# Kernel optimization log

Measured on AMD Instinct MI355X. Metric: run time of the kernel, lower is better.

## Reference

```python
import jax, jax.numpy as jnp
import numpy as np

B, N, F, S, M, K = 32, 4096, 256, 256, 1024, 11
EPS = 1e-06  # slot-attention epsilon
LN_EPS = 1e-05  # torch LayerNorm default
NUM_ITERS = 3


def _ln(x, g, b):
    mu = jnp.mean(x, axis=-1, keepdims=True)
    var = jnp.mean(jnp.square(x - mu), axis=-1, keepdims=True)
    return (x - mu) * jax.lax.rsqrt(var + LN_EPS) * g + b


def setup_inputs() -> dict:
    key = jax.random.key(0)
    ks = jax.random.split(key, 12)
    def xavier(k, shape):
        fan_in, fan_out = shape[0], shape[-1]
        lim = np.sqrt(6.0 / (fan_in + fan_out))
        return jax.random.uniform(k, shape, jnp.float32, -lim, lim)
    return {
        "features": jax.random.normal(ks[0], (B, N, F), jnp.float32),
        "sigma": jnp.array([0.1], jnp.float32),
        "z": jax.random.normal(ks[1], (B, K, S), jnp.float32),
        "slots_init_w": xavier(ks[2], (K, S)),
        "gf": jnp.ones((F,), jnp.float32), "bf": jnp.zeros((F,), jnp.float32),
        "gs": jnp.ones((S,), jnp.float32), "bs": jnp.zeros((S,), jnp.float32),
        "gm": jnp.ones((S,), jnp.float32), "bm": jnp.zeros((S,), jnp.float32),
        "Wk": xavier(ks[3], (F, S)),
        "Wv": xavier(ks[4], (F, S)),
        "Wq": xavier(ks[5], (S, S)),
        "W_ih": xavier(ks[6], (3 * S, S)),
        "W_hh": xavier(ks[7], (3 * S, S)),
        "b_ih": jnp.zeros((3 * S,), jnp.float32),
        "b_hh": jnp.zeros((3 * S,), jnp.float32),
        "W1": xavier(ks[8], (S, M)), "b1": jnp.zeros((M,), jnp.float32),
        "W2": xavier(ks[9], (M, S)), "b2": jnp.zeros((S,), jnp.float32),
    }


def _gru(x, h, W_ih, W_hh, b_ih, b_hh):
    # torch GRUCell: gates ordered (r, z, n)
    gi = x @ W_ih.T + b_ih  # [..., 3S]
    gh = h @ W_hh.T + b_hh
    ir, iz, inn = jnp.split(gi, 3, axis=-1)
    hr, hz, hn = jnp.split(gh, 3, axis=-1)
    r = jax.nn.sigmoid(ir + hr)
    zg = jax.nn.sigmoid(iz + hz)
    n = jnp.tanh(inn + r * hn)
    return (1.0 - zg) * n + zg * h


def reference(features, sigma, z, slots_init_w, gf, bf, gs, bs, gm, bm,
              Wk, Wv, Wq, W_ih, W_hh, b_ih, b_hh, W1, b1, W2, b2):
    mu = jnp.broadcast_to(slots_init_w[None], (features.shape[0], K, S))
    slots_init = mu + z * sigma * jax.lax.stop_gradient(mu)
    feats = _ln(features, gf, bf)
    k = feats @ Wk  # [B,N,S]
    v = feats @ Wv  # [B,N,S]
    D = v.shape[-1]
    scale = D ** -0.5
    slots = slots_init
    attn = None
    for i in range(NUM_ITERS):
        if i == NUM_ITERS - 1:
            slots = jax.lax.stop_gradient(slots) + slots_init - jax.lax.stop_gradient(slots_init)
        slots_prev = slots
        q = _ln(slots, gs, bs) @ Wq  # [B,K,S]
        attn_logits = jnp.einsum('bid,bjd->bij', q, k) * scale  # [B,K,N]
        attn = jax.nn.softmax(attn_logits, axis=1)  # softmax over slots axis
        attn_wm = attn / (jnp.sum(attn, axis=-1, keepdims=True) + EPS)
        updates = jnp.einsum('bij,bjd->bid', attn_wm, v)  # [B,K,S]
        slots = _gru(updates, slots_prev, W_ih, W_hh, b_ih, b_hh)
        slots = slots + (jax.nn.relu(_ln(slots, gm, bm) @ W1 + b1) @ W2 + b2)
    return slots, attn
```

## Files before the change

### kernel.cpp

```cpp
#include <hip/hip_runtime.h>

#define EPS 1e-6f
#define LN_EPS 1e-5f

typedef unsigned short u16;
typedef unsigned int u32;
typedef short bf16x8 __attribute__((ext_vector_type(8)));
typedef float f32x4 __attribute__((ext_vector_type(4)));

__device__ __forceinline__ float bf2f(u16 u) {
  return __uint_as_float(((u32)u) << 16);
}
__device__ __forceinline__ u16 f2bf(float f) {
  u32 x = __float_as_uint(f);
  x += 0x7fffu + ((x >> 16) & 1u);
  return (u16)(x >> 16);
}

__global__ void prep_kernel(const float* __restrict__ W_ih,
                            const float* __restrict__ W_hh,
                            const float* __restrict__ W1,
                            const float* __restrict__ W2,
                            const float* __restrict__ Wq,
                            const float* __restrict__ Wk,
                            const float* __restrict__ Wv,
                            const float* __restrict__ slots_init_w,
                            const float* __restrict__ z,
                            const float* __restrict__ sigma,
                            float* __restrict__ wihT, float* __restrict__ whhT,
                            short* __restrict__ W1b, short* __restrict__ W2b,
                            short* __restrict__ Wqb, short* __restrict__ Btb,
                            float* __restrict__ slots, float* __restrict__ upd,
                            float* __restrict__ sums) {
  int e = blockIdx.x * 256 + threadIdx.x;
  if (e < 196608) {
    int j = e >> 8, d = e & 255;
    wihT[d * 768 + j] = W_ih[e];
  } else if (e < 393216) {
    int e2 = e - 196608;
    int j = e2 >> 8, d = e2 & 255;
    whhT[d * 768 + j] = W_hh[e2];
  } else if (e < 655360) {
    int e2 = e - 393216;
    W1b[e2] = (short)f2bf(W1[e2]);
  } else if (e < 917504) {
    int e2 = e - 655360;
    W2b[e2] = (short)f2bf(W2[e2]);
  } else if (e < 983040) {
    int e2 = e - 917504;
    Wqb[e2] = (short)f2bf(Wq[e2]);
  } else if (e < 1114112) {
    int e2 = e - 983040;
    int f = e2 >> 9, j = e2 & 511;
    float v = (j < 256) ? Wk[f * 256 + j] : Wv[f * 256 + (j - 256)];
    Btb[j * 256 + f] = (short)f2bf(v);
  } else if (e < 1204224) {
    int i = e - 1114112;
    int s = i & 255;
    int k = (i >> 8) % 11;
    float wv = slots_init_w[k * 256 + s];
    slots[i] = wv + z[i] * sigma[0] * wv;
    upd[i] = 0.f;
    if (i < 352) sums[i] = 0.f;
  }
}

__global__ __launch_bounds__(256) void gemm_kv(
    const float* __restrict__ feat, const short* __restrict__ Btb,
    const float* __restrict__ gf, const float* __restrict__ bfp,
    short* __restrict__ knorm, short* __restrict__ vT) {
  __shared__ short As[16384];
  __shared__ short Bs[2][8192];
  int t = threadIdx.x;
  int w = t >> 6, lane = t & 63;
  int quad = lane >> 4, l16 = lane & 15;
  int i0 = blockIdx.x * 64;
  int wi = (w & 1) * 32, wj = (w >> 1) * 64;

  {
    #pragma unroll
    for (int c = 0; c < 4; ++c) {
      int lin = c * 256 + t;
      int jr = lin >> 3, p = lin & 7;
      int q = (p - jr) & 7;
      const short* gB = Btb + (long)jr * 256 + q * 8;
      __builtin_amdgcn_global_load_lds(
          (const __attribute__((address_space(1))) void*)gB,
          (__attribute__((address_space(3))) void*)&Bs[0][lin * 8], 16, 0, 0);
    }
  }

  {
    int r = t >> 2;
    int qd = t & 3;
    const float* frow = feat + (long)(i0 + r) * 256 + qd * 64;
    float4 fv[16];
    float s = 0.f, s2 = 0.f;
    #pragma unroll
    for (int i = 0; i < 16; ++i) {
      fv[i] = *(const float4*)(frow + i * 4);
      s += fv[i].x + fv[i].y + fv[i].z + fv[i].w;
      s2 += fv[i].x * fv[i].x + fv[i].y * fv[i].y + fv[i].z * fv[i].z +
            fv[i].w * fv[i].w;
    }
    s += __shfl_xor(s, 1); s2 += __shfl_xor(s2, 1);
    s += __shfl_xor(s, 2); s2 += __shfl_xor(s2, 2);
    float mu = s * (1.f / 256.f);
    float rs = rsqrtf(s2 * (1.f / 256.f) - mu * mu + LN_EPS);
    #pragma unroll
    for (int c = 0; c < 8; ++c) {
      float4 a = fv[c * 2], b = fv[c * 2 + 1];
      int fb = qd * 64 + c * 8;
      float4 g0 = *(const float4*)(gf + fb);
      float4 g1 = *(const float4*)(gf + fb + 4);
      float4 e0 = *(const float4*)(bfp + fb);
      float4 e1 = *(const float4*)(bfp + fb + 4);
      bf16x8 pk;
      pk[0] = (short)f2bf((a.x - mu) * rs * g0.x + e0.x);
      pk[1] = (short)f2bf((a.y - mu) * rs * g0.y + e0.y);
      pk[2] = (short)f2bf((a.z - mu) * rs * g0.z + e0.z);
      pk[3] = (short)f2bf((a.w - mu) * rs * g0.w + e0.w);
      pk[4] = (short)f2bf((b.x - mu) * rs * g1.x + e1.x);
      pk[5] = (short)f2bf((b.y - mu) * rs * g1.y + e1.y);
      pk[6] = (short)f2bf((b.z - mu) * rs * g1.z + e1.z);
      pk[7] = (short)f2bf((b.w - mu) * rs * g1.w + e1.w);
      int p = qd * 8 + ((c + 2 * qd + r) & 7);
      *(bf16x8*)&As[r * 256 + p * 8] = pk;
    }
  }
  __syncthreads();

  f32x4 acc[2][4];
  #pragma unroll
  for (int a = 0; a < 2; ++a)
    #pragma unroll
    for (int b = 0; b < 4; ++b) acc[a][b] = (f32x4){0.f, 0.f, 0.f, 0.f};

  for (int idx = 0; idx < 16; ++idx) {
    int jq = idx >> 2, ks = idx & 3;
    int buf = idx & 1;
    if (idx < 15) {
      int jn = (idx + 1) >> 2, kn = (idx + 1) & 3;
      #pragma unroll
      for (int c = 0; c < 4; ++c) {
        int lin = c * 256 + t;
        int jr = lin >> 3, p = lin & 7;
        int q = (p - jr) & 7;
        const short* gB = Btb + (long)(jn * 128 + jr) * 256 + kn * 64 + q * 8;
        __builtin_amdgcn_global_load_lds(
            (const __attribute__((address_space(1))) void*)gB,
            (__attribute__((address_space(3))) void*)&Bs[buf ^ 1][lin * 8],
            16, 0, 0);
      }
    }
    #pragma unroll
    for (int kh = 0; kh < 2; ++kh) {
      bf16x8 af[2], bfr[4];
      #pragma unroll
      for (int mi = 0; mi < 2; ++mi) {
        int m = wi + mi * 16 + l16;
        int p = ks * 8 + ((kh * 4 + quad + 2 * ks + m) & 7);
        af[mi] = *(const bf16x8*)&As[m * 256 + p * 8];
      }
      #pragma unroll
      for (int ni = 0; ni < 4; ++ni) {
        int j = wj + ni * 16 + l16;
        int p = ((kh * 4 + quad) + j) & 7;
        bfr[ni] = *(const bf16x8*)&Bs[buf][j * 64 + p * 8];
      }
      if (jq < 2) {
        #pragma unroll
        for (int mi = 0; mi < 2; ++mi)
          #pragma unroll
          for (int ni = 0; ni < 4; ++ni)
            acc[mi][ni] = __builtin_amdgcn_mfma_f32_16x16x32_bf16(
                bfr[ni], af[mi], acc[mi][ni], 0, 0, 0);
      } else {
        #pragma unroll
        for (int mi = 0; mi < 2; ++mi)
          #pragma unroll
          for (int ni = 0; ni < 4; ++ni)
            acc[mi][ni] = __builtin_amdgcn_mfma_f32_16x16x32_bf16(
                af[mi], bfr[ni], acc[mi][ni], 0, 0, 0);
      }
    }
    if (ks == 3) {
      if (jq < 2) {
        #pragma unroll
        for (int mi = 0; mi < 2; ++mi) {
          long i = i0 + wi + mi * 16 + l16;
          #pragma unroll
          for (int ni = 0; ni < 4; ++ni) {
            int fb = jq * 128 + wj + ni * 16 + quad * 4;
            ushort4 u;
            u.x = f2bf(acc[mi][ni][0]);
            u.y = f2bf(acc[mi][ni][1]);
            u.z = f2bf(acc[mi][ni][2]);
            u.w = f2bf(acc[mi][ni][3]);
            *(ushort4*)&knorm[i * 256 + fb] = u;
          }
        }
      } else {
        #pragma unroll
        for (int ni = 0; ni < 4; ++ni) {
          int s = (jq - 2) * 128 + wj + ni * 16 + l16;
          #pragma unroll
          for (int mi = 0; mi < 2; ++mi) {
            long ib = i0 + wi + mi * 16 + quad * 4;
            ushort4 u;
            u.x = f2bf(acc[mi][ni][0]);
            u.y = f2bf(acc[mi][ni][1]);
            u.z = f2bf(acc[mi][ni][2]);
            u.w = f2bf(acc[mi][ni][3]);
            *(ushort4*)&vT[(long)s * 131072 + ib] = u;
          }
        }
      }
      #pragma unroll
      for (int a = 0; a < 2; ++a)
        #pragma unroll
        for (int b = 0; b < 4; ++b) acc[a][b] = (f32x4){0.f, 0.f, 0.f, 0.f};
    }
    __syncthreads();
  }
}

__global__ __launch_bounds__(256) void qproj_kernel(
    const float* __restrict__ slots, const float* __restrict__ gs,
    const float* __restrict__ bs, const short* __restrict__ Wqb,
    float* __restrict__ qout) {
  __shared__ float lnq[256];
  __shared__ float red[8];
  int row = blockIdx.x, t = threadIdx.x;
  int w = t >> 6, lane = t & 63;
  float x = slots[(long)row * 256 + t];
  float s = x, s2 = x * x;
  #pragma unroll
  for (int off = 32; off > 0; off >>= 1) {
    s += __shfl_xor(s, off);
    s2 += __shfl_xor(s2, off);
  }
  if (lane == 0) { red[w * 2] = s; red[w * 2 + 1] = s2; }
  __syncthreads();
  float st = red[0] + red[2] + red[4] + red[6];
  float st2 = red[1] + red[3] + red[5] + red[7];
  float mu = st * (1.f / 256.f);
  float rs = rsqrtf(st2 * (1.f / 256.f) - mu * mu + LN_EPS);
  lnq[t] = (x - mu) * rs * gs[t] + bs[t];
  __syncthreads();
  float acc = 0.f;
  for (int k = 0; k < 256; ++k)
    acc += lnq[k] * bf2f((u16)Wqb[k * 256 + t]);
  qout[(long)row * 256 + t] = acc;
}

__global__ __launch_bounds__(256) void attn_upd(
    const float* __restrict__ q, const short* __restrict__ knorm,
    const short* __restrict__ vT, float* __restrict__ attn_out,
    float* __restrict__ sums, float* __restrict__ upd, int emit_attn) {
  __shared__ short qs[16 * 264];
  __shared__ short ps[16 * 520];
  int b = blockIdx.y;
  int n0 = blockIdx.x * 512;
  int t = threadIdx.x, lane = t & 63;
  int w = t >> 6, quad = lane >> 4, l16 = lane & 15;
  for (int e = t; e < 5 * 264; e += 256) qs[11 * 264 + e] = 0;
  for (int e = t; e < 2816; e += 256) {
    int kk = e >> 8, f = e & 255;
    qs[kk * 264 + f] = (short)f2bf(q[b * 2816 + e]);
  }
  __syncthreads();
  f32x4 acc[8];
  #pragma unroll
  for (int mi = 0; mi < 8; ++mi) acc[mi] = (f32x4){0.f, 0.f, 0.f, 0.f};
  long nbase = (long)b * 4096 + n0 + w * 128;
  const short* kb = knorm + (nbase + l16) * 256 + quad * 8;
  #pragma unroll
  for (int c = 0; c < 8; ++c) {
    bf16x8 qf = *(const bf16x8*)&qs[l16 * 264 + c * 32 + quad * 8];
    #pragma unroll
    for (int mi = 0; mi < 8; ++mi) {
      bf16x8 kf = *(const bf16x8*)&kb[mi * 16 * 256 + c * 32];
      acc[mi] = __builtin_amdgcn_mfma_f32_16x16x32_bf16(kf, qf, acc[mi], 0, 0, 0);
    }
  }
  bool valid = l16 < 11;
  float slsum = 0.f;
  #pragma unroll
  for (int mi = 0; mi < 8; ++mi) {
    float4 pv;
    #pragma unroll
    for (int r = 0; r < 4; ++r) {
      float L = acc[mi][r] * 0.0625f;
      float Lm = valid ? L : -1e30f;
      Lm = fmaxf(Lm, __shfl_xor(Lm, 1));
      Lm = fmaxf(Lm, __shfl_xor(Lm, 2));
      Lm = fmaxf(Lm, __shfl_xor(Lm, 4));
      Lm = fmaxf(Lm, __shfl_xor(Lm, 8));
      float p = valid ? expf(L - Lm) : 0.f;
      float ss = p;
      ss += __shfl_xor(ss, 1);
      ss += __shfl_xor(ss, 2);
      ss += __shfl_xor(ss, 4);
      ss += __shfl_xor(ss, 8);
      p = p / ss;
      (&pv.x)[r] = p;
      slsum += p;
      ps[l16 * 520 + w * 128 + mi * 16 + quad * 4 + r] = (short)f2bf(p);
    }
    if (emit_attn && valid)
      *(float4*)(attn_out + ((long)b * 11 + l16) * 4096 + n0 + w * 128 +
                 mi * 16 + quad * 4) = pv;
  }
  slsum += __shfl_xor(slsum, 16);
  slsum += __shfl_xor(slsum, 32);
  if (valid && quad == 0) atomicAdd(&sums[b * 11 + l16], slsum);
  __syncthreads();
  f32x4 acc4[4];
  #pragma unroll
  for (int mi = 0; mi < 4; ++mi) acc4[mi] = (f32x4){0.f, 0.f, 0.f, 0.f};
  #pragma unroll
  for (int kst = 0; kst < 16; ++kst) {
    int nb = kst * 32 + quad * 8;
    bf16x8 bps = *(const bf16x8*)&ps[l16 * 520 + nb];
    #pragma unroll
    for (int mi = 0; mi < 4; ++mi) {
      int s = (w * 4 + mi) * 16 + l16;
      bf16x8 av =
          *(const bf16x8*)&vT[(long)s * 131072 + (long)b * 4096 + n0 + nb];
      acc4[mi] =
          __builtin_amdgcn_mfma_f32_16x16x32_bf16(av, bps, acc4[mi], 0, 0, 0);
    }
  }
  if (l16 < 11) {
    #pragma unroll
    for (int mi = 0; mi < 4; ++mi) {
      int sb = (w * 4 + mi) * 16 + quad * 4;
      #pragma unroll
      for (int r = 0; r < 4; ++r)
        atomicAdd(&upd[((long)b * 11 + l16) * 256 + sb + r], acc4[mi][r]);
    }
  }
}

__global__ __launch_bounds__(256) void slot_step(
    float* __restrict__ upd, float* __restrict__ sums,
    const float* __restrict__ slots_in,
    const float* __restrict__ wihT, const float* __restrict__ whhT,
    const float* __restrict__ b_ih, const float* __restrict__ b_hh,
    const float* __restrict__ gm, const float* __restrict__ bm,
    const short* __restrict__ W1b, const float* __restrict__ b1,
    const short* __restrict__ W2b, const float* __restrict__ b2,
    const float* __restrict__ gs, const float* __restrict__ bs,
    const short* __restrict__ Wqb,
    float* __restrict__ slots_out, float* __restrict__ qout, int emit_q) {
  __shared__ float xs[2][256], hs[2][256], sgv[2][256], ln1[2][256];
  __shared__ float giv[2][768], ghv[2][768];
  __shared__ float h1v[2][1024];
  __shared__ float pw2[4][2][256];
  __shared__ float red[2][2];
  int t = threadIdx.x;
  int w = t >> 6, lane = t & 63;
  int r0 = blockIdx.x * 2;
  #pragma unroll
  for (int row = 0; row < 2; ++row) {
    int r = r0 + row;
    float sc = 1.0f / (sums[r] + EPS);
    xs[row][t] = upd[(long)r * 256 + t] * sc;
    hs[row][t] = slots_in[(long)r * 256 + t];
  }
  __syncthreads();
  #pragma unroll
  for (int row = 0; row < 2; ++row) {
    upd[(long)(r0 + row) * 256 + t] = 0.f;
    if (t == row) sums[r0 + row] = 0.f;
  }
  {
    float accI[2][3] = {}, accH[2][3] = {};
    for (int k = 0; k < 256; ++k) {
      float x0 = xs[0][k], x1 = xs[1][k];
      float h0 = hs[0][k], h1 = hs[1][k];
      #pragma unroll
      for (int j = 0; j < 3; ++j) {
        float wI = wihT[k * 768 + j * 256 + t];
        float wH = whhT[k * 768 + j * 256 + t];
        accI[0][j] += x0 * wI; accI[1][j] += x1 * wI;
        accH[0][j] += h0 * wH; accH[1][j] += h1 * wH;
      }
    }
    #pragma unroll
    for (int row = 0; row < 2; ++row)
      #pragma unroll
      for (int j = 0; j < 3; ++j) {
        giv[row][j * 256 + t] = accI[row][j] + b_ih[j * 256 + t];
        ghv[row][j * 256 + t] = accH[row][j] + b_hh[j * 256 + t];
      }
  }
  __syncthreads();
  #pragma unroll
  for (int row = 0; row < 2; ++row) {
    float irv = giv[row][t], izv = giv[row][256 + t], inv = giv[row][512 + t];
    float hrv = ghv[row][t], hzv = ghv[row][256 + t], hnv = ghv[row][512 + t];
    float hv = hs[row][t];
    float rg = 1.f / (1.f + expf(-(irv + hrv)));
    float zg = 1.f / (1.f + expf(-(izv + hzv)));
    float ng = tanhf(inv + rg * hnv);
    sgv[row][t] = (1.f - zg) * ng + zg * hv;
  }
  __syncthreads();
  if (w < 2) {
    float4 sv = *(const float4*)&sgv[w][lane * 4];
    float s = sv.x + sv.y + sv.z + sv.w;
    float s2 = sv.x * sv.x + sv.y * sv.y + sv.z * sv.z + sv.w * sv.w;
    #pragma unroll
    for (int off = 32; off > 0; off >>= 1) {
      s += __shfl_xor(s, off);
      s2 += __shfl_xor(s2, off);
    }
    if (lane == 0) {
      float mu = s * (1.f / 256.f);
      red[w][0] = mu;
      red[w][1] = rsqrtf(s2 * (1.f / 256.f) - mu * mu + LN_EPS);
    }
  }
  __syncthreads();
  #pragma unroll
  for (int row = 0; row < 2; ++row)
    ln1[row][t] = (sgv[row][t] - red[row][0]) * red[row][1] * gm[t] + bm[t];
  __syncthreads();
  {
    float acc1[2][4] = {};
    for (int k = 0; k < 256; ++k) {
      ushort4 w4 = *(const ushort4*)(W1b + (long)k * 1024 + 4 * t);
      float wv[4] = {bf2f(w4.x), bf2f(w4.y), bf2f(w4.z), bf2f(w4.w)};
      float l0 = ln1[0][k], l1 = ln1[1][k];
      #pragma unroll
      for (int j = 0; j < 4; ++j) {
        acc1[0][j] += l0 * wv[j];
        acc1[1][j] += l1 * wv[j];
      }
    }
    #pragma unroll
    for (int row = 0; row < 2; ++row)
      #pragma unroll
      for (int j = 0; j < 4; ++j)
        h1v[row][4 * t + j] = fmaxf(acc1[row][j] + b1[4 * t + j], 0.f);
  }
  __syncthreads();
  {
    float acc2[2][4] = {};
    int kbase = w * 256;
    for (int kk = 0; kk < 256; ++kk) {
      int k = kbase + kk;
      ushort4 w4 = *(const ushort4*)(W2b + (long)k * 256 + 4 * lane);
      float wv[4] = {bf2f(w4.x), bf2f(w4.y), bf2f(w4.z), bf2f(w4.w)};
      float h0 = h1v[0][k], h1 = h1v[1][k];
      #pragma unroll
      for (int j = 0; j < 4; ++j) {
        acc2[0][j] += h0 * wv[j];
        acc2[1][j] += h1 * wv[j];
      }
    }
    #pragma unroll
    for (int row = 0; row < 2; ++row)
      #pragma unroll
      for (int j = 0; j < 4; ++j) pw2[w][row][4 * lane + j] = acc2[row][j];
  }
  __syncthreads();
  float outv[2];
  #pragma unroll
  for (int row = 0; row < 2; ++row) {
    float s = pw2[0][row][t] + pw2[1][row][t] + pw2[2][row][t] + pw2[3][row][t];
    outv[row] = s + b2[t] + sgv[row][t];
    slots_out[(long)(r0 + row) * 256 + t] = outv[row];
  }
  if (emit_q) {
    __syncthreads();
    xs[0][t] = outv[0];
    xs[1][t] = outv[1];
    __syncthreads();
    if (w < 2) {
      float4 sv = *(const float4*)&xs[w][lane * 4];
      float s = sv.x + sv.y + sv.z + sv.w;
      float s2 = sv.x * sv.x + sv.y * sv.y + sv.z * sv.z + sv.w * sv.w;
      #pragma unroll
      for (int off = 32; off > 0; off >>= 1) {
        s += __shfl_xor(s, off);
        s2 += __shfl_xor(s2, off);
      }
      if (lane == 0) {
        float mu = s * (1.f / 256.f);
        red[w][0] = mu;
        red[w][1] = rsqrtf(s2 * (1.f / 256.f) - mu * mu + LN_EPS);
      }
    }
    __syncthreads();
    #pragma unroll
    for (int row = 0; row < 2; ++row)
      hs[row][t] = (xs[row][t] - red[row][0]) * red[row][1] * gs[t] + bs[t];
    __syncthreads();
    float accq[2] = {};
    for (int k = 0; k < 256; ++k) {
      float wq = bf2f((u16)Wqb[k * 256 + t]);
      accq[0] += hs[0][k] * wq;
      accq[1] += hs[1][k] * wq;
    }
    #pragma unroll
    for (int row = 0; row < 2; ++row)
      qout[(long)(r0 + row) * 256 + t] = accq[row];
  }
}

extern "C" void kernel_launch(void* const* d_in, const int* in_sizes, int n_in,
                              void* d_out, int out_size, void* d_ws,
                              size_t ws_size, hipStream_t stream) {
  const float* features = (const float*)d_in[0];
  const float* sigma = (const float*)d_in[1];
  const float* z = (const float*)d_in[2];
  const float* slots_init_w = (const float*)d_in[3];
  const float* gf = (const float*)d_in[4];
  const float* bf = (const float*)d_in[5];
  const float* gs = (const float*)d_in[6];
  const float* bs = (const float*)d_in[7];
  const float* gm = (const float*)d_in[8];
  const float* bm = (const float*)d_in[9];
  const float* Wk = (const float*)d_in[10];
  const float* Wv = (const float*)d_in[11];
  const float* Wq = (const float*)d_in[12];
  const float* W_ih = (const float*)d_in[13];
  const float* W_hh = (const float*)d_in[14];
  const float* b_ih = (const float*)d_in[15];
  const float* b_hh = (const float*)d_in[16];
  const float* W1 = (const float*)d_in[17];
  const float* b1 = (const float*)d_in[18];
  const float* W2 = (const float*)d_in[19];
  const float* b2 = (const float*)d_in[20];

  float* ws = (float*)d_ws;
  size_t o = 0;
  short* knorm = (short*)(ws + o); o += 16777216;
  short* vT = (short*)(ws + o); o += 16777216;
  short* Btb = (short*)(ws + o); o += 65536;
  float* wihT = ws + o; o += 196608;
  float* whhT = ws + o; o += 196608;
  short* W1b = (short*)(ws + o); o += 131072;
  short* W2b = (short*)(ws + o); o += 131072;
  short* Wqb = (short*)(ws + o); o += 32768;
  float* slots = ws + o; o += 90112;
  float* qbuf = ws + o; o += 90112;
  float* upd = ws + o; o += 90112;
  float* sums = ws + o; o += 352;

  float* out_slots = (float*)d_out;
  float* out_attn = (float*)d_out + 90112;

  prep_kernel<<<4704, 256, 0, stream>>>(W_ih, W_hh, W1, W2, Wq, Wk, Wv,
                                        slots_init_w, z, sigma, wihT, whhT,
                                        W1b, W2b, Wqb, Btb, slots, upd, sums);
  gemm_kv<<<2048, 256, 0, stream>>>(features, Btb, gf, bf, knorm, vT);
  qproj_kernel<<<352, 256, 0, stream>>>(slots, gs, bs, Wqb, qbuf);

  for (int it = 0; it < 3; ++it) {
    attn_upd<<<dim3(8, 32), 256, 0, stream>>>(
        qbuf, knorm, vT, out_attn, sums, upd, (it == 2) ? 1 : 0);
    slot_step<<<176, 256, 0, stream>>>(
        upd, sums, slots, wihT, whhT, b_ih, b_hh, gm, bm, W1b, b1, W2b, b2,
        gs, bs, Wqb, (it == 2) ? out_slots : slots, qbuf, (it < 2) ? 1 : 0);
  }
}
```

Baseline: 689.1 us.

## Stage K/V epilogue through LDS, fold q-projection into GEMM launch, bf16 GRU weights

The K/V GEMM epilogue now writes bf16 results into a padded LDS tile and then emits 16-byte coalesced global stores, replacing scattered 8-byte stores (notably the strided vT transpose writes). The separate q-projection kernel is removed; its work runs as 352 extra blocks of the gemm_kv launch, which saves one launch. GRU weight matrices are converted to bf16 to halve the weight bandwidth in slot_step, at some precision cost. The epilogue adds extra LDS and barriers per output tile.

```diff
diff --git a/kernel.cpp b/kernel.cpp
--- a/kernel.cpp
+++ b/kernel.cpp
@@ -27,7 +27,7 @@
                             const float* __restrict__ slots_init_w,
                             const float* __restrict__ z,
                             const float* __restrict__ sigma,
-                            float* __restrict__ wihT, float* __restrict__ whhT,
+                            short* __restrict__ wihTb, short* __restrict__ whhTb,
                             short* __restrict__ W1b, short* __restrict__ W2b,
                             short* __restrict__ Wqb, short* __restrict__ Btb,
                             float* __restrict__ slots, float* __restrict__ upd,
@@ -35,11 +35,11 @@
   int e = blockIdx.x * 256 + threadIdx.x;
   if (e < 196608) {
     int j = e >> 8, d = e & 255;
-    wihT[d * 768 + j] = W_ih[e];
+    wihTb[d * 768 + j] = (short)f2bf(W_ih[e]);
   } else if (e < 393216) {
     int e2 = e - 196608;
     int j = e2 >> 8, d = e2 & 255;
-    whhT[d * 768 + j] = W_hh[e2];
+    whhTb[d * 768 + j] = (short)f2bf(W_hh[e2]);
   } else if (e < 655360) {
     int e2 = e - 393216;
     W1b[e2] = (short)f2bf(W1[e2]);
@@ -68,12 +68,43 @@
 __global__ __launch_bounds__(256) void gemm_kv(
     const float* __restrict__ feat, const short* __restrict__ Btb,
     const float* __restrict__ gf, const float* __restrict__ bfp,
-    short* __restrict__ knorm, short* __restrict__ vT) {
+    short* __restrict__ knorm, short* __restrict__ vT,
+    const float* __restrict__ slots, const float* __restrict__ gs,
+    const float* __restrict__ bs, const short* __restrict__ Wqb,
+    float* __restrict__ qbuf) {
   __shared__ short As[16384];
   __shared__ short Bs[2][8192];
+  __shared__ short Cs[4608];
   int t = threadIdx.x;
   int w = t >> 6, lane = t & 63;
   int quad = lane >> 4, l16 = lane & 15;
+
+  if (blockIdx.x >= 2048) {
+    float* lnq = (float*)As;
+    float* red = (float*)As + 256;
+    int row = blockIdx.x - 2048;
+    float x = slots[(long)row * 256 + t];
+    float s = x, s2 = x * x;
+    #pragma unroll
+    for (int off = 32; off > 0; off >>= 1) {
+      s += __shfl_xor(s, off);
+      s2 += __shfl_xor(s2, off);
+    }
+    if (lane == 0) { red[w * 2] = s; red[w * 2 + 1] = s2; }
+    __syncthreads();
+    float st = red[0] + red[2] + red[4] + red[6];
+    float st2 = red[1] + red[3] + red[5] + red[7];
+    float mu = st * (1.f / 256.f);
+    float rs = rsqrtf(st2 * (1.f / 256.f) - mu * mu + LN_EPS);
+    lnq[t] = (x - mu) * rs * gs[t] + bs[t];
+    __syncthreads();
+    float acc = 0.f;
+    for (int k = 0; k < 256; ++k)
+      acc += lnq[k] * bf2f((u16)Wqb[k * 256 + t]);
+    qbuf[(long)row * 256 + t] = acc;
+    return;
+  }
+
   int i0 = blockIdx.x * 64;
   int wi = (w & 1) * 32, wj = (w >> 1) * 64;
 
@@ -187,33 +218,63 @@
     if (ks == 3) {
       if (jq < 2) {
         #pragma unroll
-        for (int mi = 0; mi < 2; ++mi) {
-          long i = i0 + wi + mi * 16 + l16;
+        for (int half = 0; half < 2; ++half) {
+          if ((w >> 1) == half) {
+            #pragma unroll
+            for (int mi = 0; mi < 2; ++mi) {
+              int il = wi + mi * 16 + l16;
+              #pragma unroll
+              for (int ni = 0; ni < 4; ++ni) {
+                int fw = ni * 16 + quad * 4;
+                ushort4 u;
+                u.x = f2bf(acc[mi][ni][0]);
+                u.y = f2bf(acc[mi][ni][1]);
+                u.z = f2bf(acc[mi][ni][2]);
+                u.w = f2bf(acc[mi][ni][3]);
+                *(ushort4*)&Cs[il * 72 + fw] = u;
+              }
+            }
+          }
+          __syncthreads();
           #pragma unroll
-          for (int ni = 0; ni < 4; ++ni) {
-            int fb = jq * 128 + wj + ni * 16 + quad * 4;
-            ushort4 u;
-            u.x = f2bf(acc[mi][ni][0]);
-            u.y = f2bf(acc[mi][ni][1]);
-            u.z = f2bf(acc[mi][ni][2]);
-            u.w = f2bf(acc[mi][ni][3]);
-            *(ushort4*)&knorm[i * 256 + fb] = u;
+          for (int c = 0; c < 2; ++c) {
+            int e = c * 256 + t;
+            int il = e >> 3, f8 = e & 7;
+            bf16x8 vv = *(const bf16x8*)&Cs[il * 72 + f8 * 8];
+            *(bf16x8*)&knorm[(long)(i0 + il) * 256 + jq * 128 + half * 64 +
+                             f8 * 8] = vv;
           }
+          __syncthreads();
         }
       } else {
         #pragma unroll
-        for (int ni = 0; ni < 4; ++ni) {
-          int s = (jq - 2) * 128 + wj + ni * 16 + l16;
+        for (int half = 0; half < 2; ++half) {
+          if ((w >> 1) == half) {
+            #pragma unroll
+            for (int ni = 0; ni < 4; ++ni) {
+              int sw = ni * 16 + l16;
+              #pragma unroll
+              for (int mi = 0; mi < 2; ++mi) {
+                int il = wi + mi * 16 + quad * 4;
+                ushort4 u;
+                u.x = f2bf(acc[mi][ni][0]);
+                u.y = f2bf(acc[mi][ni][1]);
+                u.z = f2bf(acc[mi][ni][2]);
+                u.w = f2bf(acc[mi][ni][3]);
+                *(ushort4*)&Cs[sw * 72 + il] = u;
+              }
+            }
+          }
+          __syncthreads();
           #pragma unroll
-          for (int mi = 0; mi < 2; ++mi) {
-            long ib = i0 + wi + mi * 16 + quad * 4;
-            ushort4 u;
-            u.x = f2bf(acc[mi][ni][0]);
-            u.y = f2bf(acc[mi][ni][1]);
-            u.z = f2bf(acc[mi][ni][2]);
-            u.w = f2bf(acc[mi][ni][3]);
-            *(ushort4*)&vT[(long)s * 131072 + ib] = u;
+          for (int c = 0; c < 2; ++c) {
+            int e = c * 256 + t;
+            int sl_ = e >> 3, i8 = e & 7;
+            bf16x8 vv = *(const bf16x8*)&Cs[sl_ * 72 + i8 * 8];
+            *(bf16x8*)&vT[(long)((jq - 2) * 128 + half * 64 + sl_) * 131072 +
+                          i0 + i8 * 8] = vv;
           }
+          __syncthreads();
         }
       }
       #pragma unroll
@@ -223,35 +284,6 @@
     }
     __syncthreads();
   }
-}
-
-__global__ __launch_bounds__(256) void qproj_kernel(
-    const float* __restrict__ slots, const float* __restrict__ gs,
-    const float* __restrict__ bs, const short* __restrict__ Wqb,
-    float* __restrict__ qout) {
-  __shared__ float lnq[256];
-  __shared__ float red[8];
-  int row = blockIdx.x, t = threadIdx.x;
-  int w = t >> 6, lane = t & 63;
-  float x = slots[(long)row * 256 + t];
-  float s = x, s2 = x * x;
-  #pragma unroll
-  for (int off = 32; off > 0; off >>= 1) {
-    s += __shfl_xor(s, off);
-    s2 += __shfl_xor(s2, off);
-  }
-  if (lane == 0) { red[w * 2] = s; red[w * 2 + 1] = s2; }
-  __syncthreads();
-  float st = red[0] + red[2] + red[4] + red[6];
-  float st2 = red[1] + red[3] + red[5] + red[7];
-  float mu = st * (1.f / 256.f);
-  float rs = rsqrtf(st2 * (1.f / 256.f) - mu * mu + LN_EPS);
-  lnq[t] = (x - mu) * rs * gs[t] + bs[t];
-  __syncthreads();
-  float acc = 0.f;
-  for (int k = 0; k < 256; ++k)
-    acc += lnq[k] * bf2f((u16)Wqb[k * 256 + t]);
-  qout[(long)row * 256 + t] = acc;
 }
 
 __global__ __launch_bounds__(256) void attn_upd(
@@ -346,7 +378,7 @@
 __global__ __launch_bounds__(256) void slot_step(
     float* __restrict__ upd, float* __restrict__ sums,
     const float* __restrict__ slots_in,
-    const float* __restrict__ wihT, const float* __restrict__ whhT,
+    const short* __restrict__ wihTb, const short* __restrict__ whhTb,
     const float* __restrict__ b_ih, const float* __restrict__ b_hh,
     const float* __restrict__ gm, const float* __restrict__ bm,
     const short* __restrict__ W1b, const float* __restrict__ b1,
@@ -382,8 +414,8 @@
       float h0 = hs[0][k], h1 = hs[1][k];
       #pragma unroll
       for (int j = 0; j < 3; ++j) {
-        float wI = wihT[k * 768 + j * 256 + t];
-        float wH = whhT[k * 768 + j * 256 + t];
+        float wI = bf2f((u16)wihTb[k * 768 + j * 256 + t]);
+        float wH = bf2f((u16)whhTb[k * 768 + j * 256 + t]);
         accI[0][j] += x0 * wI; accI[1][j] += x1 * wI;
         accH[0][j] += h0 * wH; accH[1][j] += h1 * wH;
       }
@@ -541,8 +573,8 @@
   short* knorm = (short*)(ws + o); o += 16777216;
   short* vT = (short*)(ws + o); o += 16777216;
   short* Btb = (short*)(ws + o); o += 65536;
-  float* wihT = ws + o; o += 196608;
-  float* whhT = ws + o; o += 196608;
+  short* wihTb = (short*)(ws + o); o += 98304;
+  short* whhTb = (short*)(ws + o); o += 98304;
   short* W1b = (short*)(ws + o); o += 131072;
   short* W2b = (short*)(ws + o); o += 131072;
   short* Wqb = (short*)(ws + o); o += 32768;
@@ -555,16 +587,16 @@
   float* out_attn = (float*)d_out + 90112;
 
   prep_kernel<<<4704, 256, 0, stream>>>(W_ih, W_hh, W1, W2, Wq, Wk, Wv,
-                                        slots_init_w, z, sigma, wihT, whhT,
+                                        slots_init_w, z, sigma, wihTb, whhTb,
                                         W1b, W2b, Wqb, Btb, slots, upd, sums);
-  gemm_kv<<<2048, 256, 0, stream>>>(features, Btb, gf, bf, knorm, vT);
-  qproj_kernel<<<352, 256, 0, stream>>>(slots, gs, bs, Wqb, qbuf);
+  gemm_kv<<<2400, 256, 0, stream>>>(features, Btb, gf, bf, knorm, vT,
+                                    slots, gs, bs, Wqb, qbuf);
 
   for (int it = 0; it < 3; ++it) {
     attn_upd<<<dim3(8, 32), 256, 0, stream>>>(
         qbuf, knorm, vT, out_attn, sums, upd, (it == 2) ? 1 : 0);
     slot_step<<<176, 256, 0, stream>>>(
-        upd, sums, slots, wihT, whhT, b_ih, b_hh, gm, bm, W1b, b1, W2b, b2,
+        upd, sums, slots, wihTb, whhTb, b_ih, b_hh, gm, bm, W1b, b1, W2b, b2,
         gs, bs, Wqb, (it == 2) ? out_slots : slots, qbuf, (it < 2) ? 1 : 0);
   }
 }
```

Result: slower. 804.1 us (+16.7%).

## Fuse q-projection into KV GEMM launch, split attn blocks finer, bf16 GRU weights

Applied to the files above, without the earlier changes.

Three changes. The q-projection kernel is folded into the KV GEMM launch as extra blocks, which removes one launch. attn_upd now covers 256 tokens per block instead of 512, doubling the grid to 512 blocks for better CU occupancy at the cost of more atomics. The transposed GRU weights are stored in bf16 to halve their load traffic in slot_step, which slightly reduces the precision of the GRU matmuls.

```diff
diff --git a/kernel.cpp b/kernel.cpp
--- a/kernel.cpp
+++ b/kernel.cpp
@@ -27,7 +27,7 @@
                             const float* __restrict__ slots_init_w,
                             const float* __restrict__ z,
                             const float* __restrict__ sigma,
-                            float* __restrict__ wihT, float* __restrict__ whhT,
+                            short* __restrict__ wihTb, short* __restrict__ whhTb,
                             short* __restrict__ W1b, short* __restrict__ W2b,
                             short* __restrict__ Wqb, short* __restrict__ Btb,
                             float* __restrict__ slots, float* __restrict__ upd,
@@ -35,11 +35,11 @@
   int e = blockIdx.x * 256 + threadIdx.x;
   if (e < 196608) {
     int j = e >> 8, d = e & 255;
-    wihT[d * 768 + j] = W_ih[e];
+    wihTb[d * 768 + j] = (short)f2bf(W_ih[e]);
   } else if (e < 393216) {
     int e2 = e - 196608;
     int j = e2 >> 8, d = e2 & 255;
-    whhT[d * 768 + j] = W_hh[e2];
+    whhTb[d * 768 + j] = (short)f2bf(W_hh[e2]);
   } else if (e < 655360) {
     int e2 = e - 393216;
     W1b[e2] = (short)f2bf(W1[e2]);
@@ -68,12 +68,42 @@
 __global__ __launch_bounds__(256) void gemm_kv(
     const float* __restrict__ feat, const short* __restrict__ Btb,
     const float* __restrict__ gf, const float* __restrict__ bfp,
-    short* __restrict__ knorm, short* __restrict__ vT) {
+    short* __restrict__ knorm, short* __restrict__ vT,
+    const float* __restrict__ slots, const float* __restrict__ gs,
+    const float* __restrict__ bs, const short* __restrict__ Wqb,
+    float* __restrict__ qbuf) {
   __shared__ short As[16384];
   __shared__ short Bs[2][8192];
   int t = threadIdx.x;
   int w = t >> 6, lane = t & 63;
   int quad = lane >> 4, l16 = lane & 15;
+
+  if (blockIdx.x >= 2048) {
+    float* lnq = (float*)As;
+    float* red = (float*)As + 256;
+    int row = blockIdx.x - 2048;
+    float x = slots[(long)row * 256 + t];
+    float s = x, s2 = x * x;
+    #pragma unroll
+    for (int off = 32; off > 0; off >>= 1) {
+      s += __shfl_xor(s, off);
+      s2 += __shfl_xor(s2, off);
+    }
+    if (lane == 0) { red[w * 2] = s; red[w * 2 + 1] = s2; }
+    __syncthreads();
+    float st = red[0] + red[2] + red[4] + red[6];
+    float st2 = red[1] + red[3] + red[5] + red[7];
+    float mu = st * (1.f / 256.f);
+    float rs = rsqrtf(st2 * (1.f / 256.f) - mu * mu + LN_EPS);
+    lnq[t] = (x - mu) * rs * gs[t] + bs[t];
+    __syncthreads();
+    float acc = 0.f;
+    for (int k = 0; k < 256; ++k)
+      acc += lnq[k] * bf2f((u16)Wqb[k * 256 + t]);
+    qbuf[(long)row * 256 + t] = acc;
+    return;
+  }
+
   int i0 = blockIdx.x * 64;
   int wi = (w & 1) * 32, wj = (w >> 1) * 64;
 
@@ -225,43 +255,14 @@
   }
 }
 
-__global__ __launch_bounds__(256) void qproj_kernel(
-    const float* __restrict__ slots, const float* __restrict__ gs,
-    const float* __restrict__ bs, const short* __restrict__ Wqb,
-    float* __restrict__ qout) {
-  __shared__ float lnq[256];
-  __shared__ float red[8];
-  int row = blockIdx.x, t = threadIdx.x;
-  int w = t >> 6, lane = t & 63;
-  float x = slots[(long)row * 256 + t];
-  float s = x, s2 = x * x;
-  #pragma unroll
-  for (int off = 32; off > 0; off >>= 1) {
-    s += __shfl_xor(s, off);
-    s2 += __shfl_xor(s2, off);
-  }
-  if (lane == 0) { red[w * 2] = s; red[w * 2 + 1] = s2; }
-  __syncthreads();
-  float st = red[0] + red[2] + red[4] + red[6];
-  float st2 = red[1] + red[3] + red[5] + red[7];
-  float mu = st * (1.f / 256.f);
-  float rs = rsqrtf(st2 * (1.f / 256.f) - mu * mu + LN_EPS);
-  lnq[t] = (x - mu) * rs * gs[t] + bs[t];
-  __syncthreads();
-  float acc = 0.f;
-  for (int k = 0; k < 256; ++k)
-    acc += lnq[k] * bf2f((u16)Wqb[k * 256 + t]);
-  qout[(long)row * 256 + t] = acc;
-}
-
 __global__ __launch_bounds__(256) void attn_upd(
     const float* __restrict__ q, const short* __restrict__ knorm,
     const short* __restrict__ vT, float* __restrict__ attn_out,
     float* __restrict__ sums, float* __restrict__ upd, int emit_attn) {
   __shared__ short qs[16 * 264];
-  __shared__ short ps[16 * 520];
+  __shared__ short ps[16 * 264];
   int b = blockIdx.y;
-  int n0 = blockIdx.x * 512;
+  int n0 = blockIdx.x * 256;
   int t = threadIdx.x, lane = t & 63;
   int w = t >> 6, quad = lane >> 4, l16 = lane & 15;
   for (int e = t; e < 5 * 264; e += 256) qs[11 * 264 + e] = 0;
@@ -270,16 +271,16 @@
     qs[kk * 264 + f] = (short)f2bf(q[b * 2816 + e]);
   }
   __syncthreads();
-  f32x4 acc[8];
-  #pragma unroll
-  for (int mi = 0; mi < 8; ++mi) acc[mi] = (f32x4){0.f, 0.f, 0.f, 0.f};
-  long nbase = (long)b * 4096 + n0 + w * 128;
+  f32x4 acc[4];
+  #pragma unroll
+  for (int mi = 0; mi < 4; ++mi) acc[mi] = (f32x4){0.f, 0.f, 0.f, 0.f};
+  long nbase = (long)b * 4096 + n0 + w * 64;
   const short* kb = knorm + (nbase + l16) * 256 + quad * 8;
   #pragma unroll
   for (int c = 0; c < 8; ++c) {
     bf16x8 qf = *(const bf16x8*)&qs[l16 * 264 + c * 32 + quad * 8];
     #pragma unroll
-    for (int mi = 0; mi < 8; ++mi) {
+    for (int mi = 0; mi < 4; ++mi) {
       bf16x8 kf = *(const bf16x8*)&kb[mi * 16 * 256 + c * 32];
       acc[mi] = __builtin_amdgcn_mfma_f32_16x16x32_bf16(kf, qf, acc[mi], 0, 0, 0);
     }
@@ -287,7 +288,7 @@
   bool valid = l16 < 11;
   float slsum = 0.f;
   #pragma unroll
-  for (int mi = 0; mi < 8; ++mi) {
+  for (int mi = 0; mi < 4; ++mi) {
     float4 pv;
     #pragma unroll
     for (int r = 0; r < 4; ++r) {
@@ -306,10 +307,10 @@
       p = p / ss;
       (&pv.x)[r] = p;
       slsum += p;
-      ps[l16 * 520 + w * 128 + mi * 16 + quad * 4 + r] = (short)f2bf(p);
+      ps[l16 * 264 + w * 64 + mi * 16 + quad * 4 + r] = (short)f2bf(p);
     }
     if (emit_attn && valid)
-      *(float4*)(attn_out + ((long)b * 11 + l16) * 4096 + n0 + w * 128 +
+      *(float4*)(attn_out + ((long)b * 11 + l16) * 4096 + n0 + w * 64 +
                  mi * 16 + quad * 4) = pv;
   }
   slsum += __shfl_xor(slsum, 16);
@@ -320,9 +321,9 @@
   #pragma unroll
   for (int mi = 0; mi < 4; ++mi) acc4[mi] = (f32x4){0.f, 0.f, 0.f, 0.f};
   #pragma unroll
-  for (int kst = 0; kst < 16; ++kst) {
+  for (int kst = 0; kst < 8; ++kst) {
     int nb = kst * 32 + quad * 8;
-    bf16x8 bps = *(const bf16x8*)&ps[l16 * 520 + nb];
+    bf16x8 bps = *(const bf16x8*)&ps[l16 * 264 + nb];
     #pragma unroll
     for (int mi = 0; mi < 4; ++mi) {
       int s = (w * 4 + mi) * 16 + l16;
@@ -346,7 +347,7 @@
 __global__ __launch_bounds__(256) void slot_step(
     float* __restrict__ upd, float* __restrict__ sums,
     const float* __restrict__ slots_in,
-    const float* __restrict__ wihT, const float* __restrict__ whhT,
+    const short* __restrict__ wihTb, const short* __restrict__ whhTb,
     const float* __restrict__ b_ih, const float* __restrict__ b_hh,
     const float* __restrict__ gm, const float* __restrict__ bm,
     const short* __restrict__ W1b, const float* __restrict__ b1,
@@ -382,8 +383,8 @@
       float h0 = hs[0][k], h1 = hs[1][k];
       #pragma unroll
       for (int j = 0; j < 3; ++j) {
-        float wI = wihT[k * 768 + j * 256 + t];
-        float wH = whhT[k * 768 + j * 256 + t];
+        float wI = bf2f((u16)wihTb[k * 768 + j * 256 + t]);
+        float wH = bf2f((u16)whhTb[k * 768 + j * 256 + t]);
         accI[0][j] += x0 * wI; accI[1][j] += x1 * wI;
         accH[0][j] += h0 * wH; accH[1][j] += h1 * wH;
       }
@@ -541,8 +542,8 @@
   short* knorm = (short*)(ws + o); o += 16777216;
   short* vT = (short*)(ws + o); o += 16777216;
   short* Btb = (short*)(ws + o); o += 65536;
-  float* wihT = ws + o; o += 196608;
-  float* whhT = ws + o; o += 196608;
+  short* wihTb = (short*)(ws + o); o += 98304;
+  short* whhTb = (short*)(ws + o); o += 98304;
   short* W1b = (short*)(ws + o); o += 131072;
   short* W2b = (short*)(ws + o); o += 131072;
   short* Wqb = (short*)(ws + o); o += 32768;
@@ -555,16 +556,16 @@
   float* out_attn = (float*)d_out + 90112;
 
   prep_kernel<<<4704, 256, 0, stream>>>(W_ih, W_hh, W1, W2, Wq, Wk, Wv,
-                                        slots_init_w, z, sigma, wihT, whhT,
+                                        slots_init_w, z, sigma, wihTb, whhTb,
                                         W1b, W2b, Wqb, Btb, slots, upd, sums);
-  gemm_kv<<<2048, 256, 0, stream>>>(features, Btb, gf, bf, knorm, vT);
-  qproj_kernel<<<352, 256, 0, stream>>>(slots, gs, bs, Wqb, qbuf);
+  gemm_kv<<<2400, 256, 0, stream>>>(features, Btb, gf, bf, knorm, vT,
+                                    slots, gs, bs, Wqb, qbuf);
 
   for (int it = 0; it < 3; ++it) {
-    attn_upd<<<dim3(8, 32), 256, 0, stream>>>(
+    attn_upd<<<dim3(16, 32), 256, 0, stream>>>(
         qbuf, knorm, vT, out_attn, sums, upd, (it == 2) ? 1 : 0);
     slot_step<<<176, 256, 0, stream>>>(
-        upd, sums, slots, wihT, whhT, b_ih, b_hh, gm, bm, W1b, b1, W2b, b2,
+        upd, sums, slots, wihTb, whhTb, b_ih, b_hh, gm, bm, W1b, b1, W2b, b2,
         gs, bs, Wqb, (it == 2) ? out_slots : slots, qbuf, (it < 2) ? 1 : 0);
   }
 }
```

Result: slower. 726.0 us (+5.4%).
